# Kernel optimization log

Hardware: AMD Instinct MI355X
Metric: run time of the kernel (lower is better)

Reference implementation:

```python
import jax, jax.numpy as jnp
import numpy as np
from jax import lax

B, S = 32, 256
V, D = 32000, 300   # pretrained word embeddings
P, PD = 35, 32      # pos vocab / pos embed dim (from source)
M = 66              # morph feature dim
H = 6               # LSTM units per direction -> bilstm_output_size = 12
A = 12


def _lstm(x, Wx, Wh, b, reverse=False):
    # x: [B,S,F] -> h: [B,S,H]; keras gate order i,f,c,o
    xg = x @ Wx + b  # precompute input projection once: [B,S,4H]
    def step(carry, xt):
        h, c = carry
        g = xt + h @ Wh
        i, f, cand, o = jnp.split(g, 4, axis=-1)
        c = jax.nn.sigmoid(f) * c + jax.nn.sigmoid(i) * jnp.tanh(cand)
        h = jax.nn.sigmoid(o) * jnp.tanh(c)
        return (h, c), h
    h0 = jnp.zeros((x.shape[0], Wh.shape[0]), x.dtype)
    _, hs = lax.scan(step, (h0, h0), jnp.swapaxes(xg, 0, 1), reverse=reverse)
    return jnp.swapaxes(hs, 0, 1)


def setup_inputs() -> dict:
    key = jax.random.key(0)
    ks = jax.random.split(key, 16)
    F = D + PD + M
    n = lambda k, shp, s=0.1: jax.random.normal(k, shp, dtype=jnp.float32) * s
    return {
        'words': jax.random.randint(ks[0], (B, S), 0, V),
        'pos': jax.random.randint(ks[1], (B, S), 0, P),
        'morph': jax.random.uniform(ks[2], (B, S, M), dtype=jnp.float32),
        'heads': jax.random.randint(ks[3], (B, S), 0, S),
        'word_table': n(ks[4], (V, D)),
        'pos_table': n(ks[5], (P, PD)),
        'Wx_f': n(ks[6], (F, 4 * H)), 'Wh_f': n(ks[7], (H, 4 * H)), 'b_f': jnp.zeros((4 * H,), jnp.float32),
        'Wx_b': n(ks[8], (F, 4 * H)), 'Wh_b': n(ks[9], (H, 4 * H)), 'b_b': jnp.zeros((4 * H,), jnp.float32),
        'Wu': n(ks[10], (A, A)), 'bu': jnp.zeros((A,), jnp.float32),
        'Ww': n(ks[11], (A, A)), 'bw': jnp.zeros((A,), jnp.float32),
        'v': n(ks[12], (A,)),
    }


def reference(words, pos, morph, heads, word_table, pos_table,
              Wx_f, Wh_f, b_f, Wx_b, Wh_b, b_b, Wu, bu, Ww, bw, v):
    # embed + concat -> [B,S,F]
    feats = jnp.concatenate([word_table[words], pos_table[pos], morph], axis=-1)
    # BiLSTM encoder -> [B,S,12] (dropout disabled / eval)
    hf = _lstm(feats, Wx_f, Wh_f, b_f)
    hb = _lstm(feats, Wx_b, Wh_b, b_b, reverse=True)
    repr_ = jnp.concatenate([hf, hb], axis=-1)
    # Bahdanau arc scoring, vectorized over dependant i (the tf loop):
    # scores[b,i,j] = v . tanh(u_a(repr)[b,j] + w_a(repr)[b,i])
    ua = repr_ @ Wu + bu  # head-position term (j)
    wa = repr_ @ Ww + bw  # dependant term (i)
    scores = jnp.einsum('bijd,d->bij', jnp.tanh(ua[:, None, :, :] + wa[:, :, None, :]), v)
    # the equality-based mask in tf picks out j == i (self cannot be head)
    eye = jnp.eye(S, dtype=bool)
    scores = jnp.where(eye[None], -10000.0, scores)
    # per-step sparse CE (from_logits, mean over batch), summed over i=1..S-1
    logp = jax.nn.log_softmax(scores, axis=-1)
    ce = -jnp.take_along_axis(logp, heads[:, :, None], axis=2)[..., 0]  # [B,S]
    loss = jnp.sum(jnp.mean(ce[:, 1:], axis=0))
    # parent_prob_table: exp(scores) concatenated along axis 0, i-major as in tf loop
    table = jnp.swapaxes(jnp.exp(scores[:, 1:, :]), 0, 1).reshape((S - 1) * B, S)
    return loss, table
```

## Files before the change

kernel.cpp:

```cpp
#include <hip/hip_runtime.h>
#include <hip/hip_bf16.h>

#define BB 32
#define SS 256
#define DD 300
#define PDD 32
#define MM 66
#define FF 398
#define HH 6
#define G4 24
#define AA 12
#define L2E 1.4426950408889634f

__device__ __forceinline__ float fast_rcp(float x) { return __builtin_amdgcn_rcpf(x); }
__device__ __forceinline__ float bcast_lane(float x, int l) {
    return __int_as_float(__builtin_amdgcn_readlane(__float_as_int(x), l));
}
template<int CTRL>
__device__ __forceinline__ float quad_bcast(float v) {
    return __int_as_float(__builtin_amdgcn_mov_dpp(__float_as_int(v), CTRL, 0xf, 0xf, true));
}

#define EPB 32
__global__ __launch_bounds__(256) void k_embed_proj(
    const int* __restrict__ words, const int* __restrict__ pos,
    const float* __restrict__ morph, const float* __restrict__ wtab,
    const float* __restrict__ ptab,
    const float* __restrict__ Wxf, const float* __restrict__ bfv,
    const float* __restrict__ Wxb, const float* __restrict__ bbv,
    float* __restrict__ xgf, float* __restrict__ xgb)
{
    __shared__ float4 sF[100][33];
    __shared__ float4 sW[48 * 100];
    int t  = threadIdx.x;
    int p0 = blockIdx.x * EPB;

    for (int idx = t; idx < EPB * 75; idx += 256) {
        int p = idx / 75, q = idx % 75;
        sF[q][p] = *(const float4*)(wtab + (size_t)words[p0 + p] * DD + 4 * q);
    }
    {
        int idx = t;
        int p = idx / 8, q = idx % 8;
        sF[75 + q][p] = *(const float4*)(ptab + pos[p0 + p] * PDD + 4 * q);
    }
    for (int idx = t; idx < EPB * 17; idx += 256) {
        int p = idx / 17, mq = idx % 17;
        const float2* ms = (const float2*)(morph + (size_t)(p0 + p) * MM);
        float2 lo = ms[2 * mq];
        float2 hi = (mq < 16) ? ms[2 * mq + 1] : make_float2(0.f, 0.f);
        sF[83 + mq][p] = make_float4(lo.x, lo.y, hi.x, hi.y);
    }
    {
        float* sWf = (float*)sW;
        for (int idx = t; idx < FF * G4; idx += 256) {
            int k = idx / G4, j = idx % G4;
            sWf[j * 400 + k]        = Wxf[idx];
            sWf[(24 + j) * 400 + k] = Wxb[idx];
        }
        if (t < 2 * G4) {
            int j = t >> 1, k = 398 + (t & 1);
            sWf[j * 400 + k] = 0.f; sWf[(24 + j) * 400 + k] = 0.f;
        }
    }
    __syncthreads();

    int lane = t & 63, w = t >> 6;
    int p    = lane & 31;
    int cg   = w * 2 + (lane >> 5);
    int dir  = cg >> 2;
    int tg   = cg & 3;
    int j0   = tg * 6;
    const float4* wc = sW + (dir * 24 + j0) * 100;

    float a0 = 0.f, a1 = 0.f, a2 = 0.f, a3 = 0.f, a4 = 0.f, a5 = 0.f;
    #pragma unroll 4
    for (int q = 0; q < 100; ++q) {
        float4 f = sF[q][p];
        float4 w0 = wc[0 * 100 + q], w1 = wc[1 * 100 + q], w2 = wc[2 * 100 + q];
        float4 w3 = wc[3 * 100 + q], w4 = wc[4 * 100 + q], w5 = wc[5 * 100 + q];
        a0 = fmaf(f.x, w0.x, a0); a0 = fmaf(f.y, w0.y, a0);
        a0 = fmaf(f.z, w0.z, a0); a0 = fmaf(f.w, w0.w, a0);
        a1 = fmaf(f.x, w1.x, a1); a1 = fmaf(f.y, w1.y, a1);
        a1 = fmaf(f.z, w1.z, a1); a1 = fmaf(f.w, w1.w, a1);
        a2 = fmaf(f.x, w2.x, a2); a2 = fmaf(f.y, w2.y, a2);
        a2 = fmaf(f.z, w2.z, a2); a2 = fmaf(f.w, w2.w, a2);
        a3 = fmaf(f.x, w3.x, a3); a3 = fmaf(f.y, w3.y, a3);
        a3 = fmaf(f.z, w3.z, a3); a3 = fmaf(f.w, w3.w, a3);
        a4 = fmaf(f.x, w4.x, a4); a4 = fmaf(f.y, w4.y, a4);
        a4 = fmaf(f.z, w4.z, a4); a4 = fmaf(f.w, w4.w, a4);
        a5 = fmaf(f.x, w5.x, a5); a5 = fmaf(f.y, w5.y, a5);
        a5 = fmaf(f.z, w5.z, a5); a5 = fmaf(f.w, w5.w, a5);
    }

    float kk = (tg == 2) ? 2.f * L2E : -L2E;
    const float* bias = dir ? bbv : bfv;
    float* o = (dir ? xgb : xgf) + (size_t)(p0 + p) * G4 + j0;
    o[0] = (a0 + bias[j0 + 0]) * kk; o[1] = (a1 + bias[j0 + 1]) * kk;
    o[2] = (a2 + bias[j0 + 2]) * kk; o[3] = (a3 + bias[j0 + 3]) * kk;
    o[4] = (a4 + bias[j0 + 4]) * kk; o[5] = (a5 + bias[j0 + 5]) * kk;
}

__global__ __launch_bounds__(128) void k_lstm_uawa(
    const float* __restrict__ xgf, const float* __restrict__ xgb,
    const float* __restrict__ Whf, const float* __restrict__ Whb,
    const float* __restrict__ Wu, const float* __restrict__ bu,
    const float* __restrict__ Ww, const float* __restrict__ bw,
    float* __restrict__ ua, float* __restrict__ wa)
{
    __shared__ float sxg[2][(SS + 8) * G4];
    __shared__ float hbuf[2][SS * HH];
    int b    = blockIdx.x;
    int lane = threadIdx.x & 63;
    int dir  = __builtin_amdgcn_readfirstlane(threadIdx.x >> 6);

    const float* xg = (dir ? xgb : xgf) + (size_t)b * SS * G4;
    const float* Wh = dir ? Whb : Whf;

    {
        const float4* src = (const float4*)xg;
        float4* dst = (float4*)sxg[dir];
        #pragma unroll
        for (int u = 0; u < 24; ++u) {
            int d = lane + u * 64;
            int row = d / 6, c4 = d - row * 6;
            int drow = dir ? (SS - 1 - row) : row;
            dst[drow * 6 + c4] = src[d];
        }
        for (int g2 = lane; g2 < 8 * G4; g2 += 64) sxg[dir][SS * G4 + g2] = 0.f;
    }

    int g    = lane % G4;
    int cell = g >> 2;
    int type = g & 3;
    int j    = type * HH + cell;

    float kk = (type == 2) ? 2.f * L2E : -L2E;
    float wh[HH];
    #pragma unroll
    for (int m = 0; m < HH; ++m) wh[m] = Wh[m * G4 + j] * kk;
    float Bc = (type == 2) ? 1.f : 0.f;
    float Ac = (type == 2) ? -1.f : 1.f;

    float sh[HH];
    #pragma unroll
    for (int m = 0; m < HH; ++m) sh[m] = 0.f;
    float c = 0.f;
    bool wr = (lane < G4) && ((lane & 3) == 0);

    const float* xb = sxg[dir] + j;
    float* hb = hbuf[dir];

    float pg[4];
    #pragma unroll
    for (int sl = 0; sl < 4; ++sl) pg[sl] = xb[sl * G4];

    #pragma unroll 1
    for (int t = 0; t < SS; t += 4) {
        #pragma unroll
        for (int sl = 0; sl < 4; ++sl) {
            float x = pg[sl];
            pg[sl] = xb[(t + 4 + sl) * G4];

            float aa  = fmaf(sh[1], wh[1], fmaf(sh[0], wh[0], x));
            float bb2 = fmaf(sh[3], wh[3], sh[2] * wh[2]);
            float cc2 = fmaf(sh[5], wh[5], sh[4] * wh[4]);
            x = (aa + bb2) + cc2;

            float e   = __builtin_amdgcn_exp2f(x);
            float val = fmaf(Bc, e, Ac) * fast_rcp(1.f + e);

            float vi = quad_bcast<0>(val);
            float vf = quad_bcast<85>(val);
            float vc = quad_bcast<170>(val);
            float vo = quad_bcast<255>(val);

            c = fmaf(vf, c, vi * vc);
            float ec = __builtin_amdgcn_exp2f(c * (2.f * L2E));
            float h  = (ec - 1.f) * fast_rcp(ec + 1.f) * vo;

            if (wr) hb[(t + sl) * HH + cell] = h;
            #pragma unroll
            for (int m = 0; m < HH; ++m) sh[m] = bcast_lane(h, 4 * m);
        }
    }
    __syncthreads();

    #pragma unroll
    for (int half = 0; half < 2; ++half) {
        int s = (int)threadIdx.x + half * 128;
        float r[AA];
        #pragma unroll
        for (int cc = 0; cc < HH; ++cc) {
            r[cc]      = hbuf[0][s * HH + cc];
            r[HH + cc] = hbuf[1][(SS - 1 - s) * HH + cc];
        }
        float au[AA], aw[AA];
        #pragma unroll
        for (int d = 0; d < AA; ++d) { au[d] = bu[d]; aw[d] = bw[d]; }
        #pragma unroll
        for (int e2 = 0; e2 < AA; ++e2) {
            #pragma unroll
            for (int d = 0; d < AA; ++d) {
                au[d] = fmaf(r[e2], Wu[e2 * AA + d], au[d]);
                aw[d] = fmaf(r[e2], Ww[e2 * AA + d], aw[d]);
            }
        }
        float* ou = ua + ((size_t)b * SS + s) * AA;
        float* ow = wa + ((size_t)b * SS + s) * AA;
        #pragma unroll
        for (int d4 = 0; d4 < 3; ++d4) {
            *(float4*)(ou + 4 * d4) = make_float4(au[4*d4] * (2.f*L2E), au[4*d4+1] * (2.f*L2E),
                                                  au[4*d4+2] * (2.f*L2E), au[4*d4+3] * (2.f*L2E));
            *(float4*)(ow + 4 * d4) = make_float4(aw[4*d4] * (2.f*L2E), aw[4*d4+1] * (2.f*L2E),
                                                  aw[4*d4+2] * (2.f*L2E), aw[4*d4+3] * (2.f*L2E));
        }
    }
}

__global__ __launch_bounds__(256) void k_score(
    const float* __restrict__ ua, const float* __restrict__ wa,
    const float* __restrict__ v, const int* __restrict__ heads,
    float* __restrict__ out, float* __restrict__ ce)
{
    int blk = blockIdx.x;
    int b   = blk >> 6;
    int i0  = (blk & 63) * 4;
    int j   = threadIdx.x;
    int w   = j >> 6;

    __shared__ float swa[4][AA], sv[AA];
    __shared__ float part[4][4];
    if (j < 4 * AA) swa[j / AA][j % AA] = wa[((size_t)b * SS + i0 + j / AA) * AA + j % AA];
    if (j < AA) sv[j] = v[j];
    __syncthreads();

    float sumv = 0.f;
    #pragma unroll
    for (int d = 0; d < AA; ++d) sumv += sv[d];

    const float* uj = ua + ((size_t)b * SS + j) * AA;
    float4 u0 = *(const float4*)(uj);
    float4 u1 = *(const float4*)(uj + 4);
    float4 u2 = *(const float4*)(uj + 8);
    float us[AA] = {u0.x, u0.y, u0.z, u0.w, u1.x, u1.y, u1.z, u1.w,
                    u2.x, u2.y, u2.z, u2.w};

    float sv_[4];
    #pragma unroll
    for (int ii = 0; ii < 4; ++ii) {
        int i = i0 + ii;
        float acc = 0.f;
        #pragma unroll
        for (int d = 0; d < AA; ++d) {
            float e_d = __builtin_amdgcn_exp2f(us[d] + swa[ii][d]);
            acc = fmaf(sv[d], fast_rcp(1.f + e_d), acc);
        }
        float s = fmaf(-2.f, acc, sumv);
        if (j == i) s = -10000.f;
        sv_[ii] = s;

        float e = __builtin_amdgcn_exp2f(s * L2E);
        if (i >= 1)
            out[1 + (((size_t)(i - 1) * BB + b) * SS + j)] = e;

        float r = e;
        #pragma unroll
        for (int off = 32; off > 0; off >>= 1) r += __shfl_xor(r, off, 64);
        if ((j & 63) == 0) part[ii][w] = r;
    }
    __syncthreads();

    #pragma unroll
    for (int ii = 0; ii < 4; ++ii) {
        int i = i0 + ii;
        float tot = part[ii][0] + part[ii][1] + part[ii][2] + part[ii][3];
        if (j == heads[b * SS + i])
            ce[b * SS + i] = (i >= 1) ? (__logf(tot) - sv_[ii]) : 0.f;
    }
}

__global__ __launch_bounds__(256) void k_loss(const float* __restrict__ ce,
                                              float* __restrict__ out)
{
    __shared__ float red[256];
    int t = threadIdx.x;
    float a = 0.f;
    for (int k = t; k < BB * SS; k += 256) a += ce[k];
    red[t] = a; __syncthreads();
    for (int off = 128; off > 0; off >>= 1) {
        if (t < off) red[t] += red[t + off];
        __syncthreads();
    }
    if (t == 0) out[0] = red[0] * (1.f / BB);
}

extern "C" void kernel_launch(void* const* d_in, const int* in_sizes, int n_in,
                              void* d_out, int out_size, void* d_ws, size_t ws_size,
                              hipStream_t stream)
{
    const int*   words = (const int*)  d_in[0];
    const int*   pos   = (const int*)  d_in[1];
    const float* morph = (const float*)d_in[2];
    const int*   heads = (const int*)  d_in[3];
    const float* wtab  = (const float*)d_in[4];
    const float* ptab  = (const float*)d_in[5];
    const float* Wxf   = (const float*)d_in[6];
    const float* Whf   = (const float*)d_in[7];
    const float* bf    = (const float*)d_in[8];
    const float* Wxb   = (const float*)d_in[9];
    const float* Whb   = (const float*)d_in[10];
    const float* bb    = (const float*)d_in[11];
    const float* Wu    = (const float*)d_in[12];
    const float* bu    = (const float*)d_in[13];
    const float* Ww    = (const float*)d_in[14];
    const float* bw    = (const float*)d_in[15];
    const float* v     = (const float*)d_in[16];
    float* out = (float*)d_out;

    float* xgf  = (float*)d_ws;
    float* xgb  = xgf  + (size_t)BB*SS*G4;
    float* ua   = xgb  + (size_t)BB*SS*G4;
    float* wa   = ua   + (size_t)BB*SS*AA;
    float* ce   = wa   + (size_t)BB*SS*AA;

    k_embed_proj<<<(BB * SS) / EPB, 256, 0, stream>>>(words, pos, morph, wtab, ptab,
                                                      Wxf, bf, Wxb, bb, xgf, xgb);
    k_lstm_uawa<<<BB, 128, 0, stream>>>(xgf, xgb, Whf, Whb, Wu, bu, Ww, bw, ua, wa);
    k_score<<<BB * (SS / 4), 256, 0, stream>>>(ua, wa, v, heads, out, ce);
    k_loss<<<1, 256, 0, stream>>>(ce, out);
}
```

Baseline: 72.57 us.

## Fuse loss reduction into score kernel and retile embed projection with padded weights

Removes the separate single-block loss kernel by having the last-finishing score block, found through an atomic counter that the LSTM kernel resets, perform the final reduction. This saves one kernel launch and its gap. The embed projection is remapped so each thread computes 3 output columns for 2 positions instead of 6 columns for 1, and the weight rows in LDS are padded to a stride of 101 float4 to avoid bank conflicts. The cost is a threadfence and an atomic in every score block.

```diff
diff --git a/kernel.cpp b/kernel.cpp
--- a/kernel.cpp
+++ b/kernel.cpp
@@ -31,7 +31,7 @@
     float* __restrict__ xgf, float* __restrict__ xgb)
 {
     __shared__ float4 sF[100][33];
-    __shared__ float4 sW[48 * 100];
+    __shared__ float4 sW[48 * 101];
     int t  = threadIdx.x;
     int p0 = blockIdx.x * EPB;
 
@@ -55,50 +55,54 @@
         float* sWf = (float*)sW;
         for (int idx = t; idx < FF * G4; idx += 256) {
             int k = idx / G4, j = idx % G4;
-            sWf[j * 400 + k]        = Wxf[idx];
-            sWf[(24 + j) * 400 + k] = Wxb[idx];
+            sWf[j * 404 + k]        = Wxf[idx];
+            sWf[(24 + j) * 404 + k] = Wxb[idx];
         }
         if (t < 2 * G4) {
             int j = t >> 1, k = 398 + (t & 1);
-            sWf[j * 400 + k] = 0.f; sWf[(24 + j) * 400 + k] = 0.f;
-        }
-    }
-    __syncthreads();
-
-    int lane = t & 63, w = t >> 6;
-    int p    = lane & 31;
-    int cg   = w * 2 + (lane >> 5);
-    int dir  = cg >> 2;
-    int tg   = cg & 3;
-    int j0   = tg * 6;
-    const float4* wc = sW + (dir * 24 + j0) * 100;
-
-    float a0 = 0.f, a1 = 0.f, a2 = 0.f, a3 = 0.f, a4 = 0.f, a5 = 0.f;
+            sWf[j * 404 + k] = 0.f; sWf[(24 + j) * 404 + k] = 0.f;
+        }
+    }
+    __syncthreads();
+
+    int cg = t & 15;
+    int pp = t >> 4;
+    int c0 = 3 * cg;
+    int dir = c0 >= 24 ? 1 : 0;
+    int jj  = c0 - dir * 24;
+    const float4* W0 = sW + (size_t)(dir * 24 + jj + 0) * 101;
+    const float4* W1 = sW + (size_t)(dir * 24 + jj + 1) * 101;
+    const float4* W2 = sW + (size_t)(dir * 24 + jj + 2) * 101;
+
+    float a00 = 0.f, a01 = 0.f, a02 = 0.f;
+    float a10 = 0.f, a11 = 0.f, a12 = 0.f;
     #pragma unroll 4
     for (int q = 0; q < 100; ++q) {
-        float4 f = sF[q][p];
-        float4 w0 = wc[0 * 100 + q], w1 = wc[1 * 100 + q], w2 = wc[2 * 100 + q];
-        float4 w3 = wc[3 * 100 + q], w4 = wc[4 * 100 + q], w5 = wc[5 * 100 + q];
-        a0 = fmaf(f.x, w0.x, a0); a0 = fmaf(f.y, w0.y, a0);
-        a0 = fmaf(f.z, w0.z, a0); a0 = fmaf(f.w, w0.w, a0);
-        a1 = fmaf(f.x, w1.x, a1); a1 = fmaf(f.y, w1.y, a1);
-        a1 = fmaf(f.z, w1.z, a1); a1 = fmaf(f.w, w1.w, a1);
-        a2 = fmaf(f.x, w2.x, a2); a2 = fmaf(f.y, w2.y, a2);
-        a2 = fmaf(f.z, w2.z, a2); a2 = fmaf(f.w, w2.w, a2);
-        a3 = fmaf(f.x, w3.x, a3); a3 = fmaf(f.y, w3.y, a3);
-        a3 = fmaf(f.z, w3.z, a3); a3 = fmaf(f.w, w3.w, a3);
-        a4 = fmaf(f.x, w4.x, a4); a4 = fmaf(f.y, w4.y, a4);
-        a4 = fmaf(f.z, w4.z, a4); a4 = fmaf(f.w, w4.w, a4);
-        a5 = fmaf(f.x, w5.x, a5); a5 = fmaf(f.y, w5.y, a5);
-        a5 = fmaf(f.z, w5.z, a5); a5 = fmaf(f.w, w5.w, a5);
-    }
-
-    float kk = (tg == 2) ? 2.f * L2E : -L2E;
+        float4 f0 = sF[q][pp];
+        float4 f1 = sF[q][pp + 16];
+        float4 w0 = W0[q], w1 = W1[q], w2 = W2[q];
+        a00 = fmaf(f0.x, w0.x, a00); a00 = fmaf(f0.y, w0.y, a00);
+        a00 = fmaf(f0.z, w0.z, a00); a00 = fmaf(f0.w, w0.w, a00);
+        a01 = fmaf(f0.x, w1.x, a01); a01 = fmaf(f0.y, w1.y, a01);
+        a01 = fmaf(f0.z, w1.z, a01); a01 = fmaf(f0.w, w1.w, a01);
+        a02 = fmaf(f0.x, w2.x, a02); a02 = fmaf(f0.y, w2.y, a02);
+        a02 = fmaf(f0.z, w2.z, a02); a02 = fmaf(f0.w, w2.w, a02);
+        a10 = fmaf(f1.x, w0.x, a10); a10 = fmaf(f1.y, w0.y, a10);
+        a10 = fmaf(f1.z, w0.z, a10); a10 = fmaf(f1.w, w0.w, a10);
+        a11 = fmaf(f1.x, w1.x, a11); a11 = fmaf(f1.y, w1.y, a11);
+        a11 = fmaf(f1.z, w1.z, a11); a11 = fmaf(f1.w, w1.w, a11);
+        a12 = fmaf(f1.x, w2.x, a12); a12 = fmaf(f1.y, w2.y, a12);
+        a12 = fmaf(f1.z, w2.z, a12); a12 = fmaf(f1.w, w2.w, a12);
+    }
+
+    float kk = (jj >= 12 && jj < 18) ? 2.f * L2E : -L2E;
     const float* bias = dir ? bbv : bfv;
-    float* o = (dir ? xgb : xgf) + (size_t)(p0 + p) * G4 + j0;
-    o[0] = (a0 + bias[j0 + 0]) * kk; o[1] = (a1 + bias[j0 + 1]) * kk;
-    o[2] = (a2 + bias[j0 + 2]) * kk; o[3] = (a3 + bias[j0 + 3]) * kk;
-    o[4] = (a4 + bias[j0 + 4]) * kk; o[5] = (a5 + bias[j0 + 5]) * kk;
+    float b0 = bias[jj], b1 = bias[jj + 1], b2 = bias[jj + 2];
+    float* xg = dir ? xgb : xgf;
+    float* o0 = xg + (size_t)(p0 + pp) * G4 + jj;
+    float* o1 = xg + (size_t)(p0 + pp + 16) * G4 + jj;
+    o0[0] = (a00 + b0) * kk; o0[1] = (a01 + b1) * kk; o0[2] = (a02 + b2) * kk;
+    o1[0] = (a10 + b0) * kk; o1[1] = (a11 + b1) * kk; o1[2] = (a12 + b2) * kk;
 }
 
 __global__ __launch_bounds__(128) void k_lstm_uawa(
@@ -106,7 +110,7 @@
     const float* __restrict__ Whf, const float* __restrict__ Whb,
     const float* __restrict__ Wu, const float* __restrict__ bu,
     const float* __restrict__ Ww, const float* __restrict__ bw,
-    float* __restrict__ ua, float* __restrict__ wa)
+    float* __restrict__ ua, float* __restrict__ wa, int* __restrict__ cnt)
 {
     __shared__ float sxg[2][(SS + 8) * G4];
     __shared__ float hbuf[2][SS * HH];
@@ -114,6 +118,8 @@
     int lane = threadIdx.x & 63;
     int dir  = __builtin_amdgcn_readfirstlane(threadIdx.x >> 6);
 
+    if (b == 0 && threadIdx.x == 0) *cnt = 0;
+
     const float* xg = (dir ? xgb : xgf) + (size_t)b * SS * G4;
     const float* Wh = dir ? Whb : Whf;
 
@@ -221,7 +227,7 @@
 __global__ __launch_bounds__(256) void k_score(
     const float* __restrict__ ua, const float* __restrict__ wa,
     const float* __restrict__ v, const int* __restrict__ heads,
-    float* __restrict__ out, float* __restrict__ ce)
+    float* __restrict__ out, float* __restrict__ ce, int* __restrict__ cnt)
 {
     int blk = blockIdx.x;
     int b   = blk >> 6;
@@ -231,6 +237,7 @@
 
     __shared__ float swa[4][AA], sv[AA];
     __shared__ float part[4][4];
+    __shared__ int lastFlag;
     if (j < 4 * AA) swa[j / AA][j % AA] = wa[((size_t)b * SS + i0 + j / AA) * AA + j % AA];
     if (j < AA) sv[j] = v[j];
     __syncthreads();
@@ -278,21 +285,26 @@
         if (j == heads[b * SS + i])
             ce[b * SS + i] = (i >= 1) ? (__logf(tot) - sv_[ii]) : 0.f;
     }
-}
-
-__global__ __launch_bounds__(256) void k_loss(const float* __restrict__ ce,
-                                              float* __restrict__ out)
-{
-    __shared__ float red[256];
-    int t = threadIdx.x;
-    float a = 0.f;
-    for (int k = t; k < BB * SS; k += 256) a += ce[k];
-    red[t] = a; __syncthreads();
-    for (int off = 128; off > 0; off >>= 1) {
-        if (t < off) red[t] += red[t + off];
-        __syncthreads();
-    }
-    if (t == 0) out[0] = red[0] * (1.f / BB);
+
+    __threadfence();
+    __syncthreads();
+    if (j == 0) {
+        int vdone = atomicAdd(cnt, 1);
+        lastFlag = (vdone == (int)gridDim.x - 1);
+    }
+    __syncthreads();
+    if (lastFlag) {
+        __threadfence();
+        __shared__ float red[256];
+        float a = 0.f;
+        for (int k = j; k < BB * SS; k += 256) a += ce[k];
+        red[j] = a; __syncthreads();
+        for (int off = 128; off > 0; off >>= 1) {
+            if (j < off) red[j] += red[j + off];
+            __syncthreads();
+        }
+        if (j == 0) out[0] = red[0] * (1.f / BB);
+    }
 }
 
 extern "C" void kernel_launch(void* const* d_in, const int* in_sizes, int n_in,
@@ -323,10 +335,10 @@
     float* ua   = xgb  + (size_t)BB*SS*G4;
     float* wa   = ua   + (size_t)BB*SS*AA;
     float* ce   = wa   + (size_t)BB*SS*AA;
+    int*   cnt  = (int*)(ce + (size_t)BB*SS);
 
     k_embed_proj<<<(BB * SS) / EPB, 256, 0, stream>>>(words, pos, morph, wtab, ptab,
                                                       Wxf, bf, Wxb, bb, xgf, xgb);
-    k_lstm_uawa<<<BB, 128, 0, stream>>>(xgf, xgb, Whf, Whb, Wu, bu, Ww, bw, ua, wa);
-    k_score<<<BB * (SS / 4), 256, 0, stream>>>(ua, wa, v, heads, out, ce);
-    k_loss<<<1, 256, 0, stream>>>(ce, out);
-}
+    k_lstm_uawa<<<BB, 128, 0, stream>>>(xgf, xgb, Whf, Whb, Wu, bu, Ww, bw, ua, wa, cnt);
+    k_score<<<BB * (SS / 4), 256, 0, stream>>>(ua, wa, v, heads, out, ce, cnt);
+}
```

Measured after the change: 225.6 us. +210.9%, slower.
